# Kernel tuning notes

Hardware: AMD Instinct MI355X
Metric: run time of the kernel (lower is better)

Reference implementation:

```python
import jax, jax.numpy as jnp
import numpy as np
from jax import lax

NC = 10        # tess_size
EPS = 1e-07


def cpab_basis(nc):
    # Constraint matrix L @ Avees = 0, Avees = [a0,b0,a1,b1,...] per cell.
    # Continuity at interior knots x_i = i/nc, plus zero-boundary v(0)=v(1)=0.
    L = np.zeros((nc + 1, 2 * nc))
    for i in range(1, nc):
        xi = i / nc
        L[i - 1, 2 * (i - 1):2 * i] = [xi, 1.0]
        L[i - 1, 2 * i:2 * i + 2] = [-xi, -1.0]
    L[nc - 1, 1] = 1.0                      # v(0) = b_0 = 0
    L[nc, 2 * nc - 2:2 * nc] = [1.0, 1.0]   # v(1) = a_{nc-1} + b_{nc-1} = 0
    U, S, Vh = np.linalg.svd(L)
    rank = int((S > 1e-8 * S[0]).sum())
    return np.ascontiguousarray(Vh[rank:].T).astype(np.float32)  # (2*nc, nc-1)


def mlp(x1, W0, b0, W1, b1, W2, b2, W3, b3):
    h = jax.nn.relu(x1 @ W0 + b0)
    h = jax.nn.relu(h @ W1 + b1)
    h = jax.nn.relu(h @ W2 + b2)
    return h @ W3 + b3


def integrate_cpab(x, A, nc):
    # x: [N] in (0,1); A: [N, nc, 2] per-cell (slope a, intercept b).
    # Closed-form integration of dphi/dt = a_c*phi + b_c for t in [0,1],
    # walking across cells. Also accumulates s = integral of a(phi(t)) dt,
    # so dphi/dx = exp(s)  (space gradient of the transform).
    a_all = A[..., 0]
    b_all = A[..., 1]
    fnc = jnp.asarray(nc, x.dtype)
    c0 = jnp.clip(jnp.floor(x * nc).astype(jnp.int32), 0, nc - 1)

    def step(carry, _):
        phi, c, t, s, done = carry
        a = jnp.take_along_axis(a_all, c[:, None], 1)[:, 0]
        b = jnp.take_along_axis(b_all, c[:, None], 1)[:, 0]
        v = a * phi + b
        big = jnp.abs(a) > 1e-10
        a_safe = jnp.where(big, a, 1.0)
        # closed-form solution with remaining time t
        psi = jnp.where(big, (phi + b / a_safe) * jnp.exp(a * t) - b / a_safe,
                        phi + b * t)
        lo = c.astype(x.dtype) / fnc
        hi = (c + 1).astype(x.dtype) / fnc
        inside = (psi >= lo) & (psi <= hi)
        xc = jnp.where(v >= 0, hi, lo)          # boundary hit in flow direction
        vb = a * xc + b
        v_safe = jnp.where(v == 0, 1.0, v)
        ratio = jnp.maximum(vb / v_safe, 1e-30)
        t_hit = jnp.where(big, jnp.log(ratio) / a_safe, (xc - phi) / v_safe)
        act = ~done
        cross = act & ~inside
        s = s + jnp.where(act, a * jnp.where(inside, t, t_hit), 0.0)
        phi = jnp.where(cross, xc, jnp.where(act & inside, psi, phi))
        t = jnp.where(cross, t - t_hit, t)
        c = jnp.clip(jnp.where(cross, c + jnp.where(v >= 0, 1, -1), c), 0, nc - 1)
        done = done | inside
        return (phi, c, t, s, done), None

    init = (x, c0, jnp.ones_like(x), jnp.zeros_like(x),
            jnp.zeros(x.shape, bool))
    (phi, _, _, s, _), _ = lax.scan(step, init, None, length=nc + 1)
    return phi, jnp.exp(s)


def _forward(x, B, W0, b0, W1, b1, W2, b2, W3, b3):
    mask = jnp.array([1, 0])  # left=True
    x = jnp.clip(x, EPS, 1.0 - EPS)
    xm = x[:, mask]
    x1, x2 = xm[:, :1], xm[:, 1:]          # [N,1] each
    theta = mlp(x1, W0, b0, W1, b1, W2, b2, W3, b3)   # [N, nc-1]
    A = (theta @ B.T).reshape(-1, NC, 2)    # per-cell (a, b)
    z2, dz2 = integrate_cpab(x2[:, 0], A, NC)
    z = jnp.column_stack([x1[:, 0], z2])[:, mask]
    log_dz_dx = jnp.column_stack([jnp.zeros_like(x1[:, 0]),
                                  jnp.log(dz2)])[:, mask]
    return z, log_dz_dx


def setup_inputs() -> dict:
    key = jax.random.key(0)
    ks = jax.random.split(key, 9)
    N, H, D = 4_194_304, 10, NC - 1
    x = jax.random.uniform(ks[0], (N, 2), jnp.float32)
    sc = 0.5
    return {
        'x': x,
        'B': jnp.asarray(cpab_basis(NC)),
        'W0': jax.random.normal(ks[1], (1, H), jnp.float32) * sc,
        'b0': jax.random.normal(ks[2], (H,), jnp.float32) * 0.1,
        'W1': jax.random.normal(ks[3], (H, H), jnp.float32) * sc,
        'b1': jax.random.normal(ks[4], (H,), jnp.float32) * 0.1,
        'W2': jax.random.normal(ks[5], (H, H), jnp.float32) * sc,
        'b2': jax.random.normal(ks[6], (H,), jnp.float32) * 0.1,
        'W3': jax.random.normal(ks[7], (H, D), jnp.float32) * sc,
        'b3': jax.random.normal(ks[8], (D,), jnp.float32) * 0.1,
    }


def reference(x, B, W0, b0, W1, b1, W2, b2, W3, b3):
    return _forward(x, B, W0, b0, W1, b1, W2, b2, W3, b3)
```

## Files before the change

### kernel.cpp

```cpp
#include <hip/hip_runtime.h>
#include <math.h>

#define NCELL 10
#define TPTS  512
#define BLK   1024
#define GRID  512
#define PCOLS 13

__device__ __forceinline__ float satf(float v) {
    return fminf(fmaxf(v, -3.389e38f), 3.389e38f);
}

__global__ __launch_bounds__(256) void table_kernel(
    const float* __restrict__ B,
    const float* __restrict__ W0, const float* __restrict__ b0,
    const float* __restrict__ W1, const float* __restrict__ b1,
    const float* __restrict__ W2, const float* __restrict__ b2,
    const float* __restrict__ W3, const float* __restrict__ b3,
    float2* __restrict__ tabP, float lo, float hi, float dx)
{
    const int i = blockIdx.x * 256 + threadIdx.x;
    if (i >= TPTS) return;
    float x1 = fmaf((float)i, dx, lo);
    if (i == TPTS - 1) x1 = hi;

    float h0[10], h1[10], h2[10];
    #pragma unroll
    for (int j = 0; j < 10; ++j)
        h0[j] = fmaxf(fmaf(x1, W0[j], b0[j]), 0.0f);
    #pragma unroll
    for (int j = 0; j < 10; ++j) {
        float acc = b1[j];
        #pragma unroll
        for (int k = 0; k < 10; ++k) acc = fmaf(h0[k], W1[k * 10 + j], acc);
        h1[j] = fmaxf(acc, 0.0f);
    }
    #pragma unroll
    for (int j = 0; j < 10; ++j) {
        float acc = b2[j];
        #pragma unroll
        for (int k = 0; k < 10; ++k) acc = fmaf(h1[k], W2[k * 10 + j], acc);
        h2[j] = fmaxf(acc, 0.0f);
    }
    float theta[9];
    #pragma unroll
    for (int j = 0; j < 9; ++j) {
        float acc = b3[j];
        #pragma unroll
        for (int k = 0; k < 10; ++k) acc = fmaf(h2[k], W3[k * 9 + j], acc);
        theta[j] = acc;
    }
    #pragma unroll
    for (int j = 1; j <= 9; ++j) {
        float aj = 0.f, bj = 0.f;
        #pragma unroll
        for (int q = 0; q < 9; ++q) {
            aj = fmaf(theta[q], B[(2 * j) * 9 + q], aj);
            bj = fmaf(theta[q], B[(2 * j + 1) * 9 + q], bj);
        }
        const float val = fmaf(aj, (float)j / 10.0f, bj);
        float2* P = tabP + (j - 1) * TPTS;
        P[i].x = val;
        if (i > 0) P[i - 1].y = val;
    }
}

__global__ __launch_bounds__(BLK) void cpab_kernel(
    const float* __restrict__ x,
    const float* __restrict__ tabP,
    float* __restrict__ out, int N,
    float lo, float inv_dx)
{
    __shared__ float2 sT[PCOLS * TPTS];

    const int tid = threadIdx.x;

    {
        const float4* g4 = reinterpret_cast<const float4*>(tabP);
        float4* s4 = reinterpret_cast<float4*>(sT);
        const int real_lo = 2 * TPTS * 2 / 4;
        const int real_hi = 11 * TPTS * 2 / 4;
        #pragma unroll
        for (int k = tid; k < PCOLS * TPTS * 2 / 4; k += BLK) {
            const bool real = (k >= real_lo) && (k < real_hi);
            s4[k] = real ? g4[k - real_lo] : make_float4(0.f, 0.f, 0.f, 0.f);
        }
    }
    __syncthreads();

    const float hi_clip = 1.0f - 1e-7f;

    for (int i = blockIdx.x * BLK + tid; i < N; i += GRID * BLK) {
        const float2 xv = reinterpret_cast<const float2*>(x)[i];
        const float x2 = fminf(fmaxf(xv.x, 1e-7f), hi_clip);
        const float x1 = fminf(fmaxf(xv.y, 1e-7f), hi_clip);

        const float tt  = (x1 - lo) * inv_dx;
        const int  cell = min((int)tt, TPTS - 2);
        const float f   = tt - (float)cell;

        const float2* baseP = sT + cell;
        auto node = [&](int j) -> float {
            const float2 pr = baseP[(j + 1) * TPTS];
            return fmaf(f, pr.y - pr.x, pr.x);
        };

        const float p10  = x2 * 10.0f;
        const int   cc0  = (int)p10;
        const float frac = p10 - (float)cc0;
        const float nc = node(cc0);
        const float nn = node(cc0 + 1);
        const float a0s = (nn - nc) * 10.0f;
        const float u0 = fmaf(nn - nc, frac, nc);
        const bool  right = (u0 >= 0.0f);
        const float d10   = right ? 10.0f : -10.0f;
        const int   dint  = right ? 1 : -1;

        float p  = x2;
        float u  = u0;
        float ru = __builtin_amdgcn_rcpf(u0);
        int   cn = cc0 + (right ? 1 : 0);
        float w  = right ? nn : nc;
        float wnext = node(cn + dint);
        float t  = 1.0f;
        float a  = 0.0f, ra = 1.0f;
        bool  big = false;

        #pragma unroll 1
        for (int it = 0; ; ++it) {
            a   = (w - u) * d10;
            big = fabsf(a) > 1e-10f;
            ra  = __builtin_amdgcn_rcpf(big ? a : 1.0f);
            const float q  = w * ru;
            const float lg = __logf(q);
            const float xc = (float)cn * 0.1f;
            const float t_hit = big ? (lg * ra) : ((xc - p) * ru);
            if (!(t_hit < t) || it >= 11) break;
            t  -= t_hit;
            p   = xc;
            u   = w;
            ru  = __builtin_amdgcn_rcpf(w);
            cn += dint;
            w   = wnext;
            wnext = node(cn + dint);
        }

        const float e   = __expf(a * t);
        float phi = big ? fmaf(u * ra, e - 1.0f, p) : fmaf(u, t, p);
        const float ru0 = __builtin_amdgcn_rcpf(u0);
        float ldz = __logf(fabsf(u * e * ru0));
        if (u0 == 0.0f) { phi = x2; ldz = a0s; }

        reinterpret_cast<float2*>(out)[i] = make_float2(satf(phi), x1);
        reinterpret_cast<float2*>(out + (size_t)2 * N)[i] = make_float2(satf(ldz), 0.0f);
    }
}

extern "C" void kernel_launch(void* const* d_in, const int* in_sizes, int n_in,
                              void* d_out, int out_size, void* d_ws, size_t ws_size,
                              hipStream_t stream) {
    (void)n_in; (void)out_size; (void)ws_size;
    const float* x  = (const float*)d_in[0];
    const float* B  = (const float*)d_in[1];
    const float* W0 = (const float*)d_in[2];
    const float* b0 = (const float*)d_in[3];
    const float* W1 = (const float*)d_in[4];
    const float* b1 = (const float*)d_in[5];
    const float* W2 = (const float*)d_in[6];
    const float* b2 = (const float*)d_in[7];
    const float* W3 = (const float*)d_in[8];
    const float* b3 = (const float*)d_in[9];
    float2* wsP = (float2*)d_ws;
    float* out = (float*)d_out;

    const int N = in_sizes[0] / 2;
    const float lo = 1e-7f, hi = 1.0f - 1e-7f;
    const float dx = (hi - lo) / (float)(TPTS - 1);
    const float inv_dx = (float)(TPTS - 1) / (hi - lo);

    table_kernel<<<(TPTS + 255) / 256, 256, 0, stream>>>(
        B, W0, b0, W1, b1, W2, b2, W3, b3, wsP, lo, hi, dx);
    cpab_kernel<<<GRID, BLK, 0, stream>>>(
        x, (const float*)wsP, out, N, lo, inv_dx);
}
```

Before: 121.3 us.

## Process two points per thread with predicated interleaved cell-walk loops

Each thread now handles two points loaded as a float4 and runs their cell-crossing walks together in one predicated loop, exiting only when no lane in the wave still has an active walk. The aim is more independent work per thread to hide LDS and transcendental latency, plus wider global loads and stores. The trade-off is more registers, a loop that always runs to the longer of the two walks, and an extra node lookup every step. It also sets a minimum-occupancy launch bound and handles an odd trailing element separately.

Result: no change. 120.3 us, median of 2 (-0.8%).

```diff
diff --git a/kernel.cpp b/kernel.cpp
--- a/kernel.cpp
+++ b/kernel.cpp
@@ -9,6 +9,11 @@
 
 __device__ __forceinline__ float satf(float v) {
     return fminf(fmaxf(v, -3.389e38f), 3.389e38f);
+}
+
+__device__ __forceinline__ float nodef(const float2* baseP, float f, int j) {
+    const float2 pr = baseP[(j + 1) * TPTS];
+    return fmaf(f, pr.y - pr.x, pr.x);
 }
 
 __global__ __launch_bounds__(256) void table_kernel(
@@ -65,7 +70,64 @@
     }
 }
 
-__global__ __launch_bounds__(BLK) void cpab_kernel(
+#define WSTEP(S)                                                        \
+  {                                                                     \
+    const float a_n  = (w##S - u##S) * d##S;                            \
+    const bool  b_n  = fabsf(a_n) > 1e-10f;                             \
+    const float ra_n = __builtin_amdgcn_rcpf(b_n ? a_n : 1.0f);         \
+    const float q    = w##S * ru##S;                                    \
+    const float lg   = __logf(q);                                       \
+    const float xc   = (float)cn##S * 0.1f;                             \
+    const float th   = b_n ? (lg * ra_n) : ((xc - p##S) * ru##S);       \
+    a##S   = act##S ? a_n  : a##S;                                      \
+    big##S = act##S ? b_n  : big##S;                                    \
+    ra##S  = act##S ? ra_n : ra##S;                                     \
+    const bool step##S = act##S && (th < t##S) && (it < 11);            \
+    t##S  = step##S ? t##S - th : t##S;                                 \
+    p##S  = step##S ? xc : p##S;                                        \
+    u##S  = step##S ? w##S : u##S;                                      \
+    ru##S = step##S ? __builtin_amdgcn_rcpf(w##S) : ru##S;              \
+    const int cnn##S = cn##S + di##S;                                   \
+    const int cf##S  = min(max(cnn##S, -1), 11);                        \
+    const float wn##S = nodef(bP##S, f##S, cf##S);                      \
+    cn##S  = step##S ? cnn##S : cn##S;                                  \
+    w##S   = step##S ? wn##S  : w##S;                                   \
+    act##S = step##S;                                                   \
+  }
+
+#define WINIT(S, X2RAW, X1RAW)                                          \
+    const float x2##S = fminf(fmaxf(X2RAW, 1e-7f), hi_clip);            \
+    const float x1##S = fminf(fmaxf(X1RAW, 1e-7f), hi_clip);            \
+    const float tt##S = (x1##S - lo) * inv_dx;                          \
+    const int cell##S = min((int)tt##S, TPTS - 2);                      \
+    const float f##S  = tt##S - (float)cell##S;                         \
+    const float2* bP##S = sT + cell##S;                                 \
+    const float p10##S = x2##S * 10.0f;                                 \
+    const int   c0##S  = (int)p10##S;                                   \
+    const float fr##S  = p10##S - (float)c0##S;                         \
+    const float nc##S  = nodef(bP##S, f##S, c0##S);                     \
+    const float nn##S  = nodef(bP##S, f##S, c0##S + 1);                 \
+    const float a0s##S = (nn##S - nc##S) * 10.0f;                       \
+    const float u0##S  = fmaf(nn##S - nc##S, fr##S, nc##S);             \
+    const bool  r##S   = (u0##S >= 0.0f);                               \
+    const float d##S   = r##S ? 10.0f : -10.0f;                         \
+    const int   di##S  = r##S ? 1 : -1;                                 \
+    float p##S = x2##S, u##S = u0##S;                                   \
+    float ru##S = __builtin_amdgcn_rcpf(u0##S);                         \
+    int   cn##S = c0##S + (r##S ? 1 : 0);                               \
+    float w##S  = r##S ? nn##S : nc##S;                                 \
+    float t##S = 1.0f, a##S = 0.0f, ra##S = 1.0f;                       \
+    bool big##S = false, act##S = true;
+
+#define WFINI(S)                                                        \
+    const float e##S = __expf(a##S * t##S);                             \
+    float phi##S = big##S ? fmaf(u##S * ra##S, e##S - 1.0f, p##S)       \
+                          : fmaf(u##S, t##S, p##S);                     \
+    const float ru0##S = __builtin_amdgcn_rcpf(u0##S);                  \
+    float ldz##S = __logf(fabsf(u##S * e##S * ru0##S));                 \
+    if (u0##S == 0.0f) { phi##S = x2##S; ldz##S = a0s##S; }
+
+__global__ __launch_bounds__(BLK, 8) void cpab_kernel(
     const float* __restrict__ x,
     const float* __restrict__ tabP,
     float* __restrict__ out, int N,
@@ -89,70 +151,42 @@
     __syncthreads();
 
     const float hi_clip = 1.0f - 1e-7f;
-
-    for (int i = blockIdx.x * BLK + tid; i < N; i += GRID * BLK) {
+    const int pairs = N >> 1;
+
+    for (int pi = blockIdx.x * BLK + tid; pi < pairs; pi += GRID * BLK) {
+        const float4 xq = reinterpret_cast<const float4*>(x)[pi];
+        WINIT(A, xq.x, xq.y)
+        WINIT(B, xq.z, xq.w)
+
+        #pragma unroll 1
+        for (int it = 0; it < 12; ++it) {
+            if (!__any(actA || actB)) break;
+            WSTEP(A)
+            WSTEP(B)
+        }
+
+        WFINI(A)
+        WFINI(B)
+
+        reinterpret_cast<float4*>(out)[pi] =
+            make_float4(satf(phiA), x1A, satf(phiB), x1B);
+        reinterpret_cast<float4*>(out + (size_t)2 * N)[pi] =
+            make_float4(satf(ldzA), 0.0f, satf(ldzB), 0.0f);
+    }
+
+    if ((N & 1) && blockIdx.x == 0 && tid == 0) {
+        const int i = N - 1;
         const float2 xv = reinterpret_cast<const float2*>(x)[i];
-        const float x2 = fminf(fmaxf(xv.x, 1e-7f), hi_clip);
-        const float x1 = fminf(fmaxf(xv.y, 1e-7f), hi_clip);
-
-        const float tt  = (x1 - lo) * inv_dx;
-        const int  cell = min((int)tt, TPTS - 2);
-        const float f   = tt - (float)cell;
-
-        const float2* baseP = sT + cell;
-        auto node = [&](int j) -> float {
-            const float2 pr = baseP[(j + 1) * TPTS];
-            return fmaf(f, pr.y - pr.x, pr.x);
-        };
-
-        const float p10  = x2 * 10.0f;
-        const int   cc0  = (int)p10;
-        const float frac = p10 - (float)cc0;
-        const float nc = node(cc0);
-        const float nn = node(cc0 + 1);
-        const float a0s = (nn - nc) * 10.0f;
-        const float u0 = fmaf(nn - nc, frac, nc);
-        const bool  right = (u0 >= 0.0f);
-        const float d10   = right ? 10.0f : -10.0f;
-        const int   dint  = right ? 1 : -1;
-
-        float p  = x2;
-        float u  = u0;
-        float ru = __builtin_amdgcn_rcpf(u0);
-        int   cn = cc0 + (right ? 1 : 0);
-        float w  = right ? nn : nc;
-        float wnext = node(cn + dint);
-        float t  = 1.0f;
-        float a  = 0.0f, ra = 1.0f;
-        bool  big = false;
-
+        WINIT(T, xv.x, xv.y)
         #pragma unroll 1
-        for (int it = 0; ; ++it) {
-            a   = (w - u) * d10;
-            big = fabsf(a) > 1e-10f;
-            ra  = __builtin_amdgcn_rcpf(big ? a : 1.0f);
-            const float q  = w * ru;
-            const float lg = __logf(q);
-            const float xc = (float)cn * 0.1f;
-            const float t_hit = big ? (lg * ra) : ((xc - p) * ru);
-            if (!(t_hit < t) || it >= 11) break;
-            t  -= t_hit;
-            p   = xc;
-            u   = w;
-            ru  = __builtin_amdgcn_rcpf(w);
-            cn += dint;
-            w   = wnext;
-            wnext = node(cn + dint);
-        }
-
-        const float e   = __expf(a * t);
-        float phi = big ? fmaf(u * ra, e - 1.0f, p) : fmaf(u, t, p);
-        const float ru0 = __builtin_amdgcn_rcpf(u0);
-        float ldz = __logf(fabsf(u * e * ru0));
-        if (u0 == 0.0f) { phi = x2; ldz = a0s; }
-
-        reinterpret_cast<float2*>(out)[i] = make_float2(satf(phi), x1);
-        reinterpret_cast<float2*>(out + (size_t)2 * N)[i] = make_float2(satf(ldz), 0.0f);
+        for (int it = 0; it < 12; ++it) {
+            if (!actT) break;
+            WSTEP(T)
+        }
+        WFINI(T)
+        reinterpret_cast<float2*>(out)[i] = make_float2(satf(phiT), x1T);
+        reinterpret_cast<float2*>(out + (size_t)2 * N)[i] =
+            make_float2(satf(ldzT), 0.0f);
     }
 }
 
```
